# Kernel optimization log

Measured on AMD Instinct MI355X. Metric: run time of the kernel, lower is better.

## Reference

```python
import jax, jax.numpy as jnp
import numpy as np

P, O, Q, OS, M = 32, 128, 10, 256, 4
L, H, HD = 8, 16, 64
D = H * HD
DFF = 4 * D
ARIDX = 5
SEQ, HOR = 512, 256
EPS = 1e-6


def revin(x, mu, sigma, reverse):
    mu = mu[..., None]
    sg = sigma[..., None] + EPS
    return x * sg + mu if reverse else (x - mu) / sg


def update_stats(n, mu, sigma, x, mask):
    # Welford-style batched running stats; mask True = ignore.
    valid = (~mask).astype(x.dtype)
    k = valid.sum(-1)
    new_n = n + k
    safe = jnp.maximum(new_n, 1.0)
    new_mu = jnp.where(new_n > 0, (n * mu + (x * valid).sum(-1)) / safe, mu)
    M2 = n * sigma ** 2 + ((x - mu[:, None]) * (x - new_mu[:, None]) * valid).sum(-1)
    new_sigma = jnp.where(new_n > 0, jnp.sqrt(jnp.maximum(M2 / safe, 1e-12)), sigma)
    return new_n, new_mu, new_sigma


def running_stats(n, mu, sigma, patches, masks):
    # patches/masks: (B, N, P) -> scan over patch axis.
    def step(carry, pm):
        new = update_stats(carry[0], carry[1], carry[2], pm[0], pm[1])
        return new, (new[1], new[2])
    carry, (mus, sigs) = jax.lax.scan(
        step, (n, mu, sigma),
        (jnp.swapaxes(patches, 0, 1), jnp.swapaxes(masks, 0, 1)))
    return carry, jnp.swapaxes(mus, 0, 1), jnp.swapaxes(sigs, 0, 1)


def layer_norm(x, s):
    m = x.mean(-1, keepdims=True)
    v = ((x - m) ** 2).mean(-1, keepdims=True)
    return (x - m) * jax.lax.rsqrt(v + EPS) * s


def model_fwd(normed, mask, caches, prm):
    (W_in, b_in, ln1_s, Wqkv, Wo, ln2_s, W1, W2, lnf_s, Wout, Wqs) = prm
    B, N, _ = normed.shape
    feat = jnp.concatenate([normed, mask.astype(normed.dtype)], axis=-1)  # (B,N,2P)
    hdd = feat @ W_in + b_in
    new_caches = []
    for l in range(L):
        xn = layer_norm(hdd, ln1_s[l])
        qkv = (xn @ Wqkv[l]).reshape(B, N, 3, H, HD)
        q, k, v = qkv[:, :, 0], qkv[:, :, 1], qkv[:, :, 2]
        Kc = jnp.concatenate([caches[l][0], k], axis=1)
        Vc = jnp.concatenate([caches[l][1], v], axis=1)
        C = Kc.shape[1]
        off = C - N
        scores = jnp.einsum('bnhd,bmhd->bhnm', q, Kc) * (HD ** -0.5)
        allow = jnp.arange(C)[None, :] <= (jnp.arange(N)[:, None] + off)
        scores = jnp.where(allow[None, None], scores, -1e30)
        att = jax.nn.softmax(scores, axis=-1)
        out = jnp.einsum('bhnm,bmhd->bnhd', att, Vc).reshape(B, N, D) @ Wo[l]
        hdd = hdd + out
        hdd = hdd + jax.nn.gelu(layer_norm(hdd, ln2_s[l]) @ W1[l]) @ W2[l]
        new_caches.append((Kc, Vc))
    hf = layer_norm(hdd, lnf_s)
    return hf @ Wout, hf @ Wqs, new_caches


def decode(horizon, x, masks, prm):
    B, context = x.shape
    steps = (horizon - 1) // O
    npatch = context // P
    pi = x.reshape(B, npatch, P)
    pm = masks.reshape(B, npatch, P)
    z = jnp.zeros(B, x.dtype)
    (n, mu, sg), ctx_mu, ctx_sg = running_stats(z, z, z, pi, pm)
    caches = [(jnp.zeros((B, 0, H, HD), x.dtype), jnp.zeros((B, 0, H, HD), x.dtype)) for _ in range(L)]
    normed = jnp.where(pm, 0.0, revin(pi, ctx_mu, ctx_sg, False))
    no, nqs, caches = model_fwd(normed, pm, caches, prm)
    pf = revin(no, ctx_mu, ctx_sg, True).reshape(B, npatch, O, Q)
    qs = revin(nqs, ctx_mu, ctx_sg, True).reshape(B, npatch, OS, Q)[:, -1]
    ar = []
    last = pf[:, -1, :, ARIDX]
    for _ in range(steps):
        npi = last.reshape(B, M, P)
        nmask = jnp.zeros_like(npi, dtype=bool)
        (n, mu, sg), nmu, nsg = running_stats(n, mu, sg, npi, nmask)
        nnorm = revin(npi, nmu, nsg, False)
        no2, _, caches = model_fwd(nnorm, nmask, caches, prm)
        ren = revin(no2, nmu, nsg, True).reshape(B, M, O, Q)
        ar.append(ren[:, -1])
        last = ren[:, -1, :, ARIDX]
    ar_out = jnp.stack(ar, axis=1) if steps > 0 else None
    return pf, qs, ar_out


def flip_q(x):
    return jnp.concatenate([x[..., :1], x[..., 1:][..., ::-1]], axis=-1)


def compiled_decode(horizon, x, prm):
    B = x.shape[0]
    masks = jnp.zeros_like(x, dtype=bool)
    is_pos = jnp.all(x >= 0, axis=-1, keepdims=True)
    pf, qs, ar = decode(horizon, x, masks, prm)
    ff = jnp.concatenate([pf[:, -1], ar.reshape(B, -1, Q)], axis=1)
    fpf, fqs, far = decode(horizon, -x, masks, prm)
    fqs = flip_q(fqs)
    fpf = flip_q(fpf)
    fff = jnp.concatenate([fpf[:, -1], far.reshape(B, -1, Q)], axis=1)
    qs_c = (qs - fqs) / 2
    ff = (ff - fff) / 2
    idx = jnp.array([1, 2, 3, 4, 6, 7, 8, 9])
    ff = ff.at[:, :, idx].set(qs_c[:, :horizon, idx] - qs_c[:, :horizon, 5:6] + ff[:, :horizon, 5:6])
    ff = ff[:, :horizon]
    for i in [4, 3, 2, 1]:
        ff = ff.at[:, :, i].set(jnp.minimum(ff[:, :, i], ff[:, :, i + 1]))
    for i in [6, 7, 8, 9]:
        ff = ff.at[:, :, i].set(jnp.maximum(ff[:, :, i], ff[:, :, i - 1]))
    ff = jnp.where(is_pos[..., None], jnp.maximum(ff, 0.0), ff)
    return ff[..., 5], ff


def setup_inputs() -> dict:
    key = jax.random.key(0)
    ks = jax.random.split(key, 16)
    s = 0.02
    inp = {
        'inputs': jax.random.normal(ks[0], (32, SEQ, 1), dtype=jnp.float32),
        'W_in': jax.random.normal(ks[1], (2 * P, D), dtype=jnp.float32) * s,
        'b_in': jnp.zeros((D,), jnp.float32),
        'ln1_s': jnp.ones((L, D), jnp.float32),
        'Wqkv': jax.random.normal(ks[2], (L, D, 3 * D), dtype=jnp.float32) * s,
        'Wo': jax.random.normal(ks[3], (L, D, D), dtype=jnp.float32) * s,
        'ln2_s': jnp.ones((L, D), jnp.float32),
        'W1': jax.random.normal(ks[4], (L, D, DFF), dtype=jnp.float32) * s,
        'W2': jax.random.normal(ks[5], (L, DFF, D), dtype=jnp.float32) * s,
        'lnf_s': jnp.ones((D,), jnp.float32),
        'Wout': jax.random.normal(ks[6], (D, O * Q), dtype=jnp.float32) * s,
        'Wqs': jax.random.normal(ks[7], (D, OS * Q), dtype=jnp.float32) * s,
    }
    return inp


def reference(inputs, W_in, b_in, ln1_s, Wqkv, Wo, ln2_s, W1, W2, lnf_s, Wout, Wqs):
    prm = (W_in, b_in, ln1_s, Wqkv, Wo, ln2_s, W1, W2, lnf_s, Wout, Wqs)
    x = inputs[..., 0]  # squeeze(-1)
    med, _ = compiled_decode(HOR, x, prm)
    return med[..., None]  # (B, HOR, 1)
```

## Files before the change

kernel.cpp:

```cpp
#include <hip/hip_runtime.h>
#include <hip/hip_bf16.h>
#include <math.h>

#define PP 32
#define OO 128
#define QQ 10
#define MM 4
#define LL 8
#define HH 16
#define HD 64
#define DD 1024
#define DFF 4096
#define NPATCH 16
#define B2 64
#define CMAX 20
#define EPSF 1e-6f

typedef __attribute__((ext_vector_type(8))) short s16x8;
typedef __attribute__((ext_vector_type(4))) float f32x4;
typedef __hip_bfloat16 bf16;

__device__ inline float b2f(short u)
{
    return __uint_as_float(((unsigned)(unsigned short)u) << 16);
}

__device__ inline void ld_lds16(void* lds_base, const void* gaddr)
{
    __builtin_amdgcn_global_load_lds(
        (const __attribute__((address_space(1))) unsigned int*)gaddr,
        (__attribute__((address_space(3))) unsigned int*)lds_base, 16, 0, 0);
}

__global__ void stats_ctx_kernel(const float* __restrict__ x, float* __restrict__ ctx_mu,
                                 float* __restrict__ ctx_sg, float* __restrict__ ispos,
                                 float* __restrict__ normed)
{
    int b2 = blockIdx.x;
    int tid = threadIdx.x;
    float sign = (b2 < 32) ? 1.f : -1.f;
    const float* xp = x + (size_t)(b2 & 31) * 512;
    __shared__ float smu[NPATCH], ssg[NPATCH];
    if (tid == 0) {
        float n = 0.f, mu = 0.f, sg = 0.f;
        for (int t = 0; t < NPATCH; t++) {
            float s1 = 0.f;
            for (int p = 0; p < PP; p++) s1 += sign * xp[t * PP + p];
            float nn2 = n + 32.f;
            float nmu_ = (n * mu + s1) / nn2;
            float m2 = n * sg * sg;
            for (int p = 0; p < PP; p++) {
                float xv = sign * xp[t * PP + p];
                m2 += (xv - mu) * (xv - nmu_);
            }
            sg = sqrtf(fmaxf(m2 / nn2, 1e-12f));
            mu = nmu_; n = nn2;
            smu[t] = mu; ssg[t] = sg;
            ctx_mu[b2 * NPATCH + t] = mu;
            ctx_sg[b2 * NPATCH + t] = sg;
        }
        if (b2 < 32) {
            int ok = 1;
            for (int i = 0; i < 512; i++) if (xp[i] < 0.f) ok = 0;
            ispos[b2] = (float)ok;
        }
    }
    __syncthreads();
    for (int i = tid; i < 512; i += 64) {
        int t = i >> 5;
        normed[(size_t)b2 * 512 + i] = (sign * xp[i] - smu[t]) / (ssg[t] + EPSF);
    }
}

__global__ void stats_ar_kernel(const float* __restrict__ lastc, const float* __restrict__ ctx_mu,
                                const float* __restrict__ ctx_sg, float* __restrict__ nmu,
                                float* __restrict__ nsg, float* __restrict__ normed)
{
    int b2 = blockIdx.x;
    int tid = threadIdx.x;
    __shared__ float smu[MM], ssg[MM];
    const float* xp = lastc + (size_t)b2 * 128;
    if (tid == 0) {
        float n = 512.f;
        float mu = ctx_mu[b2 * NPATCH + 15];
        float sg = ctx_sg[b2 * NPATCH + 15];
        for (int t = 0; t < MM; t++) {
            float s1 = 0.f;
            for (int p = 0; p < PP; p++) s1 += xp[t * PP + p];
            float nn2 = n + 32.f;
            float nmu_ = (n * mu + s1) / nn2;
            float m2 = n * sg * sg;
            for (int p = 0; p < PP; p++) {
                float xv = xp[t * PP + p];
                m2 += (xv - mu) * (xv - nmu_);
            }
            sg = sqrtf(fmaxf(m2 / nn2, 1e-12f));
            mu = nmu_; n = nn2;
            smu[t] = mu; ssg[t] = sg;
            nmu[b2 * MM + t] = mu;
            nsg[b2 * MM + t] = sg;
        }
    }
    __syncthreads();
    for (int i = tid; i < 128; i += 64) {
        int t = i >> 5;
        normed[(size_t)b2 * 128 + i] = (xp[i] - smu[t]) / (ssg[t] + EPSF);
    }
}

__global__ __launch_bounds__(256) void embed_kernel(const float* __restrict__ normed,
                                                    const float* __restrict__ Win,
                                                    const float* __restrict__ bin,
                                                    float* __restrict__ hdd)
{
    int row = blockIdx.x;
    int tid = threadIdx.x;
    __shared__ float p[PP];
    if (tid < PP) p[tid] = normed[(size_t)row * PP + tid];
    __syncthreads();
    for (int c = tid; c < DD; c += 256) {
        float s = bin[c];
        for (int k = 0; k < PP; k++) s = fmaf(p[k], Win[k * DD + c], s);
        hdd[(size_t)row * DD + c] = s;
    }
}

__global__ __launch_bounds__(256) void layernorm_kernel(const float* __restrict__ in,
                                                        bf16* __restrict__ out,
                                                        const float* __restrict__ scale)
{
    int wave = threadIdx.x >> 6, lane = threadIdx.x & 63;
    size_t row = (size_t)blockIdx.x * 4 + wave;
    const float* x = in + row * DD + lane * 16;
    float e[16];
    #pragma unroll
    for (int j = 0; j < 4; j++) {
        float4 t = ((const float4*)x)[j];
        e[4 * j] = t.x; e[4 * j + 1] = t.y; e[4 * j + 2] = t.z; e[4 * j + 3] = t.w;
    }
    float s = 0.f;
    #pragma unroll
    for (int i = 0; i < 16; i++) s += e[i];
    #pragma unroll
    for (int o = 32; o > 0; o >>= 1) s += __shfl_xor(s, o, 64);
    float m = s * (1.f / 1024.f);
    float vv = 0.f;
    #pragma unroll
    for (int i = 0; i < 16; i++) { float d = e[i] - m; vv = fmaf(d, d, vv); }
    #pragma unroll
    for (int o = 32; o > 0; o >>= 1) vv += __shfl_xor(vv, o, 64);
    float inv = rsqrtf(vv * (1.f / 1024.f) + EPSF);
    const float* sc = scale + lane * 16;
    union { bf16 b[16]; s16x8 v2[2]; } ob;
    #pragma unroll
    for (int j = 0; j < 4; j++) {
        float4 t = ((const float4*)sc)[j];
        ob.b[4 * j]     = __float2bfloat16((e[4 * j]     - m) * inv * t.x);
        ob.b[4 * j + 1] = __float2bfloat16((e[4 * j + 1] - m) * inv * t.y);
        ob.b[4 * j + 2] = __float2bfloat16((e[4 * j + 2] - m) * inv * t.z);
        ob.b[4 * j + 3] = __float2bfloat16((e[4 * j + 3] - m) * inv * t.w);
    }
    s16x8* op = (s16x8*)(out + row * DD + lane * 16);
    op[0] = ob.v2[0]; op[1] = ob.v2[1];
}

__global__ __launch_bounds__(256) void transpose_w(const float* __restrict__ in,
                                                   bf16* __restrict__ out,
                                                   int R, int C)
{
    __shared__ float t[32][33];
    size_t base = (size_t)blockIdx.z * R * C;
    int c0 = blockIdx.x * 32, r0 = blockIdx.y * 32;
    int tx = threadIdx.x & 31, ty = threadIdx.x >> 5;
    #pragma unroll
    for (int s = 0; s < 4; s++)
        t[ty + 8 * s][tx] = in[base + (size_t)(r0 + ty + 8 * s) * C + c0 + tx];
    __syncthreads();
    #pragma unroll
    for (int s = 0; s < 4; s++)
        out[base + (size_t)(c0 + ty + 8 * s) * R + r0 + tx] = __float2bfloat16(t[tx][ty + 8 * s]);
}

__global__ void w5_kernel(const float* __restrict__ Wout, bf16* __restrict__ w5T)
{
    int i = blockIdx.x * 256 + threadIdx.x;
    int o = i >> 10, k = i & 1023;
    w5T[i] = __float2bfloat16(Wout[(size_t)k * (OO * QQ) + o * QQ + 5]);
}

__device__ inline float gelu_tanh(float x)
{
    float x3 = x * x * x;
    float t = tanhf(0.7978845608028654f * (x + 0.044715f * x3));
    return 0.5f * x * (1.f + t);
}

template<int BM, int BN, int EP>
__global__ __launch_bounds__(256) void hgemm(const bf16* __restrict__ A,
                                             const bf16* __restrict__ BT,
                                             float* __restrict__ C,
                                             bf16* __restrict__ Cbf,
                                             bf16* __restrict__ Kc,
                                             bf16* __restrict__ Vc,
                                             int M, int N, int K, int Kpart,
                                             int nn, int koff)
{
    constexpr int FM = BM / 32 > 0 ? BM / 32 : 1;
    constexpr int FN = BN / 32;
    __shared__ __align__(16) short As[BM * 64];
    __shared__ __align__(16) short Bs[BN * 64];
    int tid = threadIdx.x;
    int lane = tid & 63, wave = tid >> 6;
    int wm = (wave >> 1) * (BM / 2), wn = (wave & 1) * (BN / 2);
    int lm = lane & 15, quad = lane >> 4;
    int row0 = blockIdx.y * BM, col0 = blockIdx.x * BN;
    int kb = blockIdx.z * Kpart, ke = kb + Kpart;
    int r8 = lane >> 3;
    int gsw = ((lane & 7) ^ r8) * 8;
    int swz = lm & 7;

    f32x4 ac[FM][FN];
    #pragma unroll
    for (int i = 0; i < FM; i++)
        #pragma unroll
        for (int j = 0; j < FN; j++) ac[i][j] = (f32x4){0.f, 0.f, 0.f, 0.f};

    for (int k0 = kb; k0 < ke; k0 += 64) {
        #pragma unroll
        for (int c = 0; c < BM / 32; c++) {
            int ch = wave + 4 * c;
            ld_lds16(&As[ch * 512], A + (size_t)(row0 + ch * 8 + r8) * K + k0 + gsw);
        }
        #pragma unroll
        for (int c = 0; c < BN / 32; c++) {
            int ch = wave + 4 * c;
            ld_lds16(&Bs[ch * 512], BT + (size_t)(col0 + ch * 8 + r8) * K + k0 + gsw);
        }
        __syncthreads();
        #pragma unroll
        for (int kk = 0; kk < 2; kk++) {
            int gq = ((kk * 4 + quad) ^ swz) * 8;
            s16x8 af[FM], bfr[FN];
            #pragma unroll
            for (int i = 0; i < FM; i++) af[i] = *(const s16x8*)&As[(wm + i * 16 + lm) * 64 + gq];
            #pragma unroll
            for (int j = 0; j < FN; j++) bfr[j] = *(const s16x8*)&Bs[(wn + j * 16 + lm) * 64 + gq];
            #pragma unroll
            for (int i = 0; i < FM; i++)
                #pragma unroll
                for (int j = 0; j < FN; j++)
                    ac[i][j] = __builtin_amdgcn_mfma_f32_16x16x32_bf16(af[i], bfr[j], ac[i][j], 0, 0, 0);
        }
        __syncthreads();
    }
    bool multi = (gridDim.z > 1);
    #pragma unroll
    for (int i = 0; i < FM; i++) {
        #pragma unroll
        for (int j = 0; j < FN; j++) {
            #pragma unroll
            for (int r = 0; r < 4; r++) {
                int rr = row0 + wm + i * 16 + quad * 4 + r;
                int cc = col0 + wn + j * 16 + lm;
                float v = ac[i][j][r];
                if (EP == 0) {
                    size_t idx = (size_t)rr * N + cc;
                    if (multi) atomicAdd(&C[idx], v); else C[idx] = v;
                } else if (EP == 1) {
                    Cbf[(size_t)rr * N + cc] = __float2bfloat16(gelu_tanh(v));
                } else if (EP == 2) {
                    atomicAdd(&C[(size_t)rr * N + cc], v);
                } else {
                    if (cc < DD) {
                        C[(size_t)rr * DD + cc] = v;
                    } else {
                        int col = cc & (DD - 1);
                        int b = rr / nn, n = rr - b * nn;
                        int h = col >> 6, hd_ = col & 63;
                        size_t dst = (((size_t)(b * HH + h)) * CMAX + koff + n) * HD + hd_;
                        if (cc < 2 * DD) Kc[dst] = __float2bfloat16(v);
                        else             Vc[dst] = __float2bfloat16(v);
                    }
                }
            }
        }
    }
}

__global__ __launch_bounds__(64) void attn_kernel(const float* __restrict__ qb,
                                                  const bf16* __restrict__ Kc,
                                                  const bf16* __restrict__ Vc,
                                                  bf16* __restrict__ outb, int Nn, int off)
{
    int gid = blockIdx.x;
    int n = gid % Nn;
    int h = (gid / Nn) & (HH - 1);
    int b = gid / (Nn * HH);
    int lane = threadIdx.x;
    int len = n + off + 1;
    const float* q = qb + ((size_t)(b * Nn + n)) * DD + h * HD;
    const bf16* Kb = Kc + ((size_t)(b * HH + h)) * CMAX * HD;
    const bf16* Vb = Vc + ((size_t)(b * HH + h)) * CMAX * HD;

    __shared__ float sq[64];
    sq[lane] = q[lane];
    __syncthreads();

    float score = -1e30f;
    if (lane < len) {
        const s16x8* kr8 = (const s16x8*)(Kb + lane * HD);
        float s = 0.f;
        #pragma unroll
        for (int c = 0; c < 8; c++) {
            s16x8 kv = kr8[c];
            #pragma unroll
            for (int j = 0; j < 8; j++) s = fmaf(sq[c * 8 + j], b2f(kv[j]), s);
        }
        score = s * 0.125f;
    }
    float mx = score;
    for (int o = 32; o > 0; o >>= 1) mx = fmaxf(mx, __shfl_xor(mx, o, 64));
    float e = (lane < len) ? expf(score - mx) : 0.f;
    float sm = e;
    for (int o = 32; o > 0; o >>= 1) sm += __shfl_xor(sm, o, 64);
    float att = e / sm;
    __shared__ float satt[64];
    satt[lane] = att;
    __syncthreads();
    float acc = 0.f;
    for (int m = 0; m < len; m++) acc = fmaf(satt[m], __bfloat162float(Vb[m * HD + lane]), acc);
    outb[((size_t)(b * Nn + n)) * DD + h * HD + lane] = __float2bfloat16(acc);
}

__global__ __launch_bounds__(128) void lnout5_kernel(const float* __restrict__ hdd,
                                                     const float* __restrict__ lnf,
                                                     const bf16* __restrict__ w5T,
                                                     const float* __restrict__ mus,
                                                     const float* __restrict__ sgs,
                                                     float* __restrict__ last, int Nn)
{
    int b2 = blockIdx.x, tid = threadIdx.x;
    const float* x = hdd + (size_t)(b2 * Nn + Nn - 1) * DD;
    __shared__ float sx[DD];
    __shared__ float red[128];
    float s = 0.f;
    for (int i = tid; i < DD; i += 128) s += x[i];
    red[tid] = s; __syncthreads();
    for (int st = 64; st > 0; st >>= 1) { if (tid < st) red[tid] += red[tid + st]; __syncthreads(); }
    float m = red[0] * (1.f / 1024.f);
    __syncthreads();
    float vv = 0.f;
    for (int i = tid; i < DD; i += 128) { float d = x[i] - m; vv = fmaf(d, d, vv); }
    red[tid] = vv; __syncthreads();
    for (int st = 64; st > 0; st >>= 1) { if (tid < st) red[tid] += red[tid + st]; __syncthreads(); }
    float inv = rsqrtf(red[0] * (1.f / 1024.f) + EPSF);
    __syncthreads();
    for (int i = tid; i < DD; i += 128) sx[i] = (x[i] - m) * inv * lnf[i];
    __syncthreads();
    const s16x8* w8 = (const s16x8*)(w5T + (size_t)tid * DD);
    float acc = 0.f;
    for (int k = 0; k < DD / 8; k++) {
        s16x8 wv = w8[k];
        #pragma unroll
        for (int j = 0; j < 8; j++) acc = fmaf(sx[k * 8 + j], b2f(wv[j]), acc);
    }
    float mu = mus[b2 * Nn + (Nn - 1)];
    float sg = sgs[b2 * Nn + (Nn - 1)];
    last[(size_t)b2 * 128 + tid] = acc * (sg + EPSF) + mu;
}

__global__ void combine_kernel(const float* __restrict__ lastc, const float* __restrict__ lasta,
                               const float* __restrict__ ispos, float* __restrict__ out)
{
    int i = blockIdx.x * 256 + threadIdx.x;
    int b = i >> 8, t = i & 255;
    float a, an;
    if (t < 128) { a = lastc[b * 128 + t];        an = lastc[(b + 32) * 128 + t]; }
    else         { a = lasta[b * 128 + t - 128];  an = lasta[(b + 32) * 128 + t - 128]; }
    float raw = (a - an) * 0.5f;
    if (ispos[b] > 0.5f) raw = fmaxf(raw, 0.f);
    out[i] = raw;
}

extern "C" void kernel_launch(void* const* d_in, const int* in_sizes, int n_in,
                              void* d_out, int out_size, void* d_ws, size_t ws_size,
                              hipStream_t stream)
{
    (void)in_sizes; (void)n_in; (void)out_size;
    const float* x     = (const float*)d_in[0];
    const float* W_in  = (const float*)d_in[1];
    const float* b_in  = (const float*)d_in[2];
    const float* ln1_s = (const float*)d_in[3];
    const float* Wqkv  = (const float*)d_in[4];
    const float* Wo    = (const float*)d_in[5];
    const float* ln2_s = (const float*)d_in[6];
    const float* W1    = (const float*)d_in[7];
    const float* W2    = (const float*)d_in[8];
    const float* lnf_s = (const float*)d_in[9];
    const float* Wout  = (const float*)d_in[10];
    float* out = (float*)d_out;

    size_t off = 0;
    auto alloc = [&](size_t bytes) {
        char* p = (char*)d_ws + off;
        off = (off + bytes + 255) & ~(size_t)255;
        return (void*)p;
    };
    float* ctx_mu = (float*)alloc(B2 * NPATCH * 4);
    float* ctx_sg = (float*)alloc(B2 * NPATCH * 4);
    float* nmu    = (float*)alloc(B2 * MM * 4);
    float* nsg    = (float*)alloc(B2 * MM * 4);
    float* ispos  = (float*)alloc(32 * 4);
    float* normed = (float*)alloc(B2 * NPATCH * PP * 4);
    float* lastc  = (float*)alloc(B2 * 128 * 4);
    float* lasta  = (float*)alloc(B2 * 128 * 4);
    float* hdd    = (float*)alloc((size_t)B2 * NPATCH * DD * 4);
    float* qb     = (float*)alloc((size_t)B2 * NPATCH * DD * 4);
    bf16* xn      = (bf16*)alloc((size_t)B2 * NPATCH * DD * 2);
    bf16* attnb   = (bf16*)alloc((size_t)B2 * NPATCH * DD * 2);
    bf16* ffnb    = (bf16*)alloc((size_t)B2 * NPATCH * DFF * 2);
    const size_t cache_l = (size_t)B2 * HH * CMAX * HD;
    bf16* kcache  = (bf16*)alloc(LL * cache_l * 2);
    bf16* vcache  = (bf16*)alloc(LL * cache_l * 2);
    bf16* w5T     = (bf16*)alloc((size_t)OO * DD * 2);

    const size_t szQKV = (size_t)DD * 3 * DD;
    const size_t szWO  = (size_t)DD * DD;
    const size_t szW1  = (size_t)DD * DFF;
    const size_t szW2  = (size_t)DFF * DD;
    const size_t WBYTES = (szQKV + szWO + szW1 + szW2) * LL * 2 + 4096;
    bool big = (off + WBYTES) <= ws_size;

    bf16 *wqkvT = nullptr, *woT = nullptr, *w1T = nullptr, *w2T = nullptr, *rot = nullptr;
    if (big) {
        wqkvT = (bf16*)alloc(LL * szQKV * 2);
        woT   = (bf16*)alloc(LL * szWO * 2);
        w1T   = (bf16*)alloc(LL * szW1 * 2);
        w2T   = (bf16*)alloc(LL * szW2 * 2);
        transpose_w<<<dim3(3072 / 32, 1024 / 32, LL), 256, 0, stream>>>(Wqkv, wqkvT, 1024, 3072);
        transpose_w<<<dim3(1024 / 32, 1024 / 32, LL), 256, 0, stream>>>(Wo, woT, 1024, 1024);
        transpose_w<<<dim3(4096 / 32, 1024 / 32, LL), 256, 0, stream>>>(W1, w1T, 1024, 4096);
        transpose_w<<<dim3(1024 / 32, 4096 / 32, LL), 256, 0, stream>>>(W2, w2T, 4096, 1024);
    } else {
        rot = (bf16*)alloc(szW1 * 2);
    }
    w5_kernel<<<(OO * DD) / 256, 256, 0, stream>>>(Wout, w5T);

    stats_ctx_kernel<<<B2, 64, 0, stream>>>(x, ctx_mu, ctx_sg, ispos, normed);
    {
        const int R = B2 * NPATCH;
        embed_kernel<<<R, 256, 0, stream>>>(normed, W_in, b_in, hdd);
        for (int l = 0; l < LL; l++) {
            bf16* kc = kcache + l * cache_l;
            bf16* vc = vcache + l * cache_l;
            layernorm_kernel<<<R / 4, 256, 0, stream>>>(hdd, xn, ln1_s + l * DD);
            bf16* bq;
            if (big) bq = wqkvT + l * szQKV;
            else { transpose_w<<<dim3(96, 32, 1), 256, 0, stream>>>(Wqkv + l * szQKV, rot, 1024, 3072); bq = rot; }
            hgemm<64, 128, 3><<<dim3(24, 16, 1), 256, 0, stream>>>(xn, bq, qb, nullptr, kc, vc,
                                                                   R, 3072, 1024, 1024, NPATCH, 0);
            attn_kernel<<<B2 * HH * NPATCH, 64, 0, stream>>>(qb, kc, vc, attnb, NPATCH, 0);
            bf16* bo;
            if (big) bo = woT + l * szWO;
            else { transpose_w<<<dim3(32, 32, 1), 256, 0, stream>>>(Wo + l * szWO, rot, 1024, 1024); bo = rot; }
            hgemm<64, 64, 2><<<dim3(16, 16, 2), 256, 0, stream>>>(attnb, bo, hdd, nullptr, nullptr, nullptr,
                                                                  R, 1024, 1024, 512, 0, 0);
            layernorm_kernel<<<R / 4, 256, 0, stream>>>(hdd, xn, ln2_s + l * DD);
            bf16* b1;
            if (big) b1 = w1T + l * szW1;
            else { transpose_w<<<dim3(128, 32, 1), 256, 0, stream>>>(W1 + l * szW1, rot, 1024, 4096); b1 = rot; }
            hgemm<64, 128, 1><<<dim3(32, 16, 1), 256, 0, stream>>>(xn, b1, nullptr, ffnb, nullptr, nullptr,
                                                                   R, 4096, 1024, 1024, 0, 0);
            bf16* bw2;
            if (big) bw2 = w2T + l * szW2;
            else { transpose_w<<<dim3(32, 128, 1), 256, 0, stream>>>(W2 + l * szW2, rot, 4096, 1024); bw2 = rot; }
            hgemm<64, 64, 2><<<dim3(16, 16, 4), 256, 0, stream>>>(ffnb, bw2, hdd, nullptr, nullptr, nullptr,
                                                                  R, 1024, 4096, 1024, 0, 0);
        }
        lnout5_kernel<<<B2, 128, 0, stream>>>(hdd, lnf_s, w5T, ctx_mu, ctx_sg, lastc, NPATCH);
    }

    stats_ar_kernel<<<B2, 64, 0, stream>>>(lastc, ctx_mu, ctx_sg, nmu, nsg, normed);
    {
        const int R = B2 * MM;
        embed_kernel<<<R, 256, 0, stream>>>(normed, W_in, b_in, hdd);
        for (int l = 0; l < LL; l++) {
            bf16* kc = kcache + l * cache_l;
            bf16* vc = vcache + l * cache_l;
            layernorm_kernel<<<R / 4, 256, 0, stream>>>(hdd, xn, ln1_s + l * DD);
            bf16* bq;
            if (big) bq = wqkvT + l * szQKV;
            else { transpose_w<<<dim3(96, 32, 1), 256, 0, stream>>>(Wqkv + l * szQKV, rot, 1024, 3072); bq = rot; }
            hgemm<32, 64, 3><<<dim3(48, 8, 1), 256, 0, stream>>>(xn, bq, qb, nullptr, kc, vc,
                                                                 R, 3072, 1024, 1024, MM, NPATCH);
            attn_kernel<<<B2 * HH * MM, 64, 0, stream>>>(qb, kc, vc, attnb, MM, NPATCH);
            bf16* bo;
            if (big) bo = woT + l * szWO;
            else { transpose_w<<<dim3(32, 32, 1), 256, 0, stream>>>(Wo + l * szWO, rot, 1024, 1024); bo = rot; }
            hgemm<32, 64, 2><<<dim3(16, 8, 2), 256, 0, stream>>>(attnb, bo, hdd, nullptr, nullptr, nullptr,
                                                                 R, 1024, 1024, 512, 0, 0);
            layernorm_kernel<<<R / 4, 256, 0, stream>>>(hdd, xn, ln2_s + l * DD);
            bf16* b1;
            if (big) b1 = w1T + l * szW1;
            else { transpose_w<<<dim3(128, 32, 1), 256, 0, stream>>>(W1 + l * szW1, rot, 1024, 4096); b1 = rot; }
            hgemm<32, 128, 1><<<dim3(32, 8, 1), 256, 0, stream>>>(xn, b1, nullptr, ffnb, nullptr, nullptr,
                                                                  R, 4096, 1024, 1024, 0, 0);
            bf16* bw2;
            if (big) bw2 = w2T + l * szW2;
            else { transpose_w<<<dim3(32, 128, 1), 256, 0, stream>>>(W2 + l * szW2, rot, 4096, 1024); bw2 = rot; }
            hgemm<32, 64, 2><<<dim3(16, 8, 4), 256, 0, stream>>>(ffnb, bw2, hdd, nullptr, nullptr, nullptr,
                                                                 R, 1024, 4096, 1024, 0, 0);
        }
        lnout5_kernel<<<B2, 128, 0, stream>>>(hdd, lnf_s, w5T, nmu, nsg, lasta, MM);
    }

    combine_kernel<<<(32 * 256) / 256, 256, 0, stream>>>(lastc, lasta, ispos, out);
}
```

Measured before the change: 1.938 ms.

## Fuse layernorm into GEMM A-loads and fold LN scales into weights

Removes the standalone layernorm kernels. A new hgemm_ln computes per-row mean and rstd inside the GEMM block and normalizes the fp32 activations on the fly while staging them to shared memory as bf16. The LN scale vectors (ln1, ln2, lnf) are folded into the transposed weight matrices during preprocessing, and the attention kernel now packs four heads per 256-thread block. This saves kernel launches and the bf16 xn round trip through memory. In exchange, every column block recomputes the row statistics and reads fp32 activations instead of bf16, so A-side traffic rises.

```diff
diff --git a/kernel.cpp b/kernel.cpp
--- a/kernel.cpp
+++ b/kernel.cpp
@@ -125,67 +125,33 @@
     }
 }
 
-__global__ __launch_bounds__(256) void layernorm_kernel(const float* __restrict__ in,
-                                                        bf16* __restrict__ out,
-                                                        const float* __restrict__ scale)
-{
-    int wave = threadIdx.x >> 6, lane = threadIdx.x & 63;
-    size_t row = (size_t)blockIdx.x * 4 + wave;
-    const float* x = in + row * DD + lane * 16;
-    float e[16];
-    #pragma unroll
-    for (int j = 0; j < 4; j++) {
-        float4 t = ((const float4*)x)[j];
-        e[4 * j] = t.x; e[4 * j + 1] = t.y; e[4 * j + 2] = t.z; e[4 * j + 3] = t.w;
-    }
-    float s = 0.f;
-    #pragma unroll
-    for (int i = 0; i < 16; i++) s += e[i];
-    #pragma unroll
-    for (int o = 32; o > 0; o >>= 1) s += __shfl_xor(s, o, 64);
-    float m = s * (1.f / 1024.f);
-    float vv = 0.f;
-    #pragma unroll
-    for (int i = 0; i < 16; i++) { float d = e[i] - m; vv = fmaf(d, d, vv); }
-    #pragma unroll
-    for (int o = 32; o > 0; o >>= 1) vv += __shfl_xor(vv, o, 64);
-    float inv = rsqrtf(vv * (1.f / 1024.f) + EPSF);
-    const float* sc = scale + lane * 16;
-    union { bf16 b[16]; s16x8 v2[2]; } ob;
-    #pragma unroll
-    for (int j = 0; j < 4; j++) {
-        float4 t = ((const float4*)sc)[j];
-        ob.b[4 * j]     = __float2bfloat16((e[4 * j]     - m) * inv * t.x);
-        ob.b[4 * j + 1] = __float2bfloat16((e[4 * j + 1] - m) * inv * t.y);
-        ob.b[4 * j + 2] = __float2bfloat16((e[4 * j + 2] - m) * inv * t.z);
-        ob.b[4 * j + 3] = __float2bfloat16((e[4 * j + 3] - m) * inv * t.w);
-    }
-    s16x8* op = (s16x8*)(out + row * DD + lane * 16);
-    op[0] = ob.v2[0]; op[1] = ob.v2[1];
-}
-
 __global__ __launch_bounds__(256) void transpose_w(const float* __restrict__ in,
                                                    bf16* __restrict__ out,
-                                                   int R, int C)
+                                                   int R, int C,
+                                                   const float* __restrict__ scl)
 {
     __shared__ float t[32][33];
     size_t base = (size_t)blockIdx.z * R * C;
     int c0 = blockIdx.x * 32, r0 = blockIdx.y * 32;
     int tx = threadIdx.x & 31, ty = threadIdx.x >> 5;
     #pragma unroll
-    for (int s = 0; s < 4; s++)
-        t[ty + 8 * s][tx] = in[base + (size_t)(r0 + ty + 8 * s) * C + c0 + tx];
+    for (int s = 0; s < 4; s++) {
+        int row = r0 + ty + 8 * s;
+        float sc = scl ? scl[(size_t)blockIdx.z * R + row] : 1.f;
+        t[ty + 8 * s][tx] = in[base + (size_t)row * C + c0 + tx] * sc;
+    }
     __syncthreads();
     #pragma unroll
     for (int s = 0; s < 4; s++)
         out[base + (size_t)(c0 + ty + 8 * s) * R + r0 + tx] = __float2bfloat16(t[tx][ty + 8 * s]);
 }
 
-__global__ void w5_kernel(const float* __restrict__ Wout, bf16* __restrict__ w5T)
+__global__ void w5_kernel(const float* __restrict__ Wout, const float* __restrict__ lnf,
+                          bf16* __restrict__ w5T)
 {
     int i = blockIdx.x * 256 + threadIdx.x;
     int o = i >> 10, k = i & 1023;
-    w5T[i] = __float2bfloat16(Wout[(size_t)k * (OO * QQ) + o * QQ + 5]);
+    w5T[i] = __float2bfloat16(Wout[(size_t)k * (OO * QQ) + o * QQ + 5] * lnf[k]);
 }
 
 __device__ inline float gelu_tanh(float x)
@@ -200,10 +166,7 @@
                                              const bf16* __restrict__ BT,
                                              float* __restrict__ C,
                                              bf16* __restrict__ Cbf,
-                                             bf16* __restrict__ Kc,
-                                             bf16* __restrict__ Vc,
-                                             int M, int N, int K, int Kpart,
-                                             int nn, int koff)
+                                             int M, int N, int K, int Kpart)
 {
     constexpr int FM = BM / 32 > 0 ? BM / 32 : 1;
     constexpr int FN = BN / 32;
@@ -253,7 +216,6 @@
         }
         __syncthreads();
     }
-    bool multi = (gridDim.z > 1);
     #pragma unroll
     for (int i = 0; i < FM; i++) {
         #pragma unroll
@@ -263,13 +225,126 @@
                 int rr = row0 + wm + i * 16 + quad * 4 + r;
                 int cc = col0 + wn + j * 16 + lm;
                 float v = ac[i][j][r];
-                if (EP == 0) {
-                    size_t idx = (size_t)rr * N + cc;
-                    if (multi) atomicAdd(&C[idx], v); else C[idx] = v;
-                } else if (EP == 1) {
+                if (EP == 1) Cbf[(size_t)rr * N + cc] = __float2bfloat16(gelu_tanh(v));
+                else         atomicAdd(&C[(size_t)rr * N + cc], v);
+            }
+        }
+    }
+}
+
+template<int BM, int BN, int EP>
+__global__ __launch_bounds__(256) void hgemm_ln(const float* __restrict__ Afp,
+                                                const bf16* __restrict__ BT,
+                                                float* __restrict__ C,
+                                                bf16* __restrict__ Cbf,
+                                                bf16* __restrict__ Kc,
+                                                bf16* __restrict__ Vc,
+                                                int M, int N, int K,
+                                                int nn, int koff)
+{
+    constexpr int FM = BM / 32 > 0 ? BM / 32 : 1;
+    constexpr int FN = BN / 32;
+    constexpr int TPR = 256 / BM;
+    constexpr int FPT = 64 / TPR;
+    __shared__ __align__(16) short As[BM * 64];
+    __shared__ __align__(16) short Bs[BN * 64];
+    __shared__ float sa[BM], sb[BM];
+    int tid = threadIdx.x;
+    int lane = tid & 63, wave = tid >> 6;
+    int wm = (wave >> 1) * (BM / 2), wn = (wave & 1) * (BN / 2);
+    int lm = lane & 15, quad = lane >> 4;
+    int row0 = blockIdx.y * BM, col0 = blockIdx.x * BN;
+    int r8 = lane >> 3;
+    int gsw = ((lane & 7) ^ r8) * 8;
+    int swz = lm & 7;
+
+    for (int r = wave; r < BM; r += 4) {
+        const float* xr = Afp + (size_t)(row0 + r) * K + lane * 16;
+        float e[16];
+        #pragma unroll
+        for (int j = 0; j < 4; j++) {
+            float4 t = ((const float4*)xr)[j];
+            e[4 * j] = t.x; e[4 * j + 1] = t.y; e[4 * j + 2] = t.z; e[4 * j + 3] = t.w;
+        }
+        float s = 0.f;
+        #pragma unroll
+        for (int i = 0; i < 16; i++) s += e[i];
+        #pragma unroll
+        for (int o = 32; o > 0; o >>= 1) s += __shfl_xor(s, o, 64);
+        float m = s * (1.f / 1024.f);
+        float vv = 0.f;
+        #pragma unroll
+        for (int i = 0; i < 16; i++) { float d = e[i] - m; vv = fmaf(d, d, vv); }
+        #pragma unroll
+        for (int o = 32; o > 0; o >>= 1) vv += __shfl_xor(vv, o, 64);
+        if (lane == 0) {
+            float inv = rsqrtf(vv * (1.f / 1024.f) + EPSF);
+            sa[r] = inv; sb[r] = -m * inv;
+        }
+    }
+    __syncthreads();
+    int arow = tid / TPR;
+    int acol = (tid % TPR) * FPT;
+    float ia = sa[arow], ib = sb[arow];
+    const float* ap = Afp + (size_t)(row0 + arow) * K + acol;
+    int g0 = (tid % TPR) * (FPT / 8);
+
+    f32x4 ac[FM][FN];
+    #pragma unroll
+    for (int i = 0; i < FM; i++)
+        #pragma unroll
+        for (int j = 0; j < FN; j++) ac[i][j] = (f32x4){0.f, 0.f, 0.f, 0.f};
+
+    for (int k0 = 0; k0 < K; k0 += 64) {
+        float4 f[FPT / 4];
+        #pragma unroll
+        for (int j = 0; j < FPT / 4; j++) f[j] = ((const float4*)(ap + k0))[j];
+        union { bf16 h[16]; s16x8 v[2]; } pk;
+        #pragma unroll
+        for (int j = 0; j < FPT / 4; j++) {
+            pk.h[4 * j + 0] = __float2bfloat16(fmaf(f[j].x, ia, ib));
+            pk.h[4 * j + 1] = __float2bfloat16(fmaf(f[j].y, ia, ib));
+            pk.h[4 * j + 2] = __float2bfloat16(fmaf(f[j].z, ia, ib));
+            pk.h[4 * j + 3] = __float2bfloat16(fmaf(f[j].w, ia, ib));
+        }
+        #pragma unroll
+        for (int g = 0; g < FPT / 8; g++) {
+            int gg = (g0 + g) ^ (arow & 7);
+            *(s16x8*)&As[arow * 64 + gg * 8] = pk.v[g];
+        }
+        #pragma unroll
+        for (int c = 0; c < BN / 32; c++) {
+            int ch = wave + 4 * c;
+            ld_lds16(&Bs[ch * 512], BT + (size_t)(col0 + ch * 8 + r8) * K + k0 + gsw);
+        }
+        __syncthreads();
+        #pragma unroll
+        for (int kk = 0; kk < 2; kk++) {
+            int gq = ((kk * 4 + quad) ^ swz) * 8;
+            s16x8 af[FM], bfr[FN];
+            #pragma unroll
+            for (int i = 0; i < FM; i++) af[i] = *(const s16x8*)&As[(wm + i * 16 + lm) * 64 + gq];
+            #pragma unroll
+            for (int j = 0; j < FN; j++) bfr[j] = *(const s16x8*)&Bs[(wn + j * 16 + lm) * 64 + gq];
+            #pragma unroll
+            for (int i = 0; i < FM; i++)
+                #pragma unroll
+                for (int j = 0; j < FN; j++)
+                    ac[i][j] = __builtin_amdgcn_mfma_f32_16x16x32_bf16(af[i], bfr[j], ac[i][j], 0, 0, 0);
+        }
+        __syncthreads();
+    }
+    #pragma unroll
+    for (int i = 0; i < FM; i++) {
+        #pragma unroll
+        for (int j = 0; j < FN; j++) {
+            #pragma unroll
+            for (int r = 0; r < 4; r++) {
+                int rr = row0 + wm + i * 16 + quad * 4 + r;
+                int cc = col0 + wn + j * 16 + lm;
+                float v = ac[i][j][r];
+                if (EP == 1) {
                     Cbf[(size_t)rr * N + cc] = __float2bfloat16(gelu_tanh(v));
-                } else if (EP == 2) {
-                    atomicAdd(&C[(size_t)rr * N + cc], v);
                 } else {
                     if (cc < DD) {
                         C[(size_t)rr * DD + cc] = v;
@@ -287,23 +362,24 @@
     }
 }
 
-__global__ __launch_bounds__(64) void attn_kernel(const float* __restrict__ qb,
-                                                  const bf16* __restrict__ Kc,
-                                                  const bf16* __restrict__ Vc,
-                                                  bf16* __restrict__ outb, int Nn, int off)
-{
-    int gid = blockIdx.x;
+__global__ __launch_bounds__(256) void attn_kernel(const float* __restrict__ qb,
+                                                   const bf16* __restrict__ Kc,
+                                                   const bf16* __restrict__ Vc,
+                                                   bf16* __restrict__ outb, int Nn, int off)
+{
+    int wave = threadIdx.x >> 6, lane = threadIdx.x & 63;
+    int gid = blockIdx.x * 4 + wave;
     int n = gid % Nn;
     int h = (gid / Nn) & (HH - 1);
     int b = gid / (Nn * HH);
-    int lane = threadIdx.x;
     int len = n + off + 1;
     const float* q = qb + ((size_t)(b * Nn + n)) * DD + h * HD;
     const bf16* Kb = Kc + ((size_t)(b * HH + h)) * CMAX * HD;
     const bf16* Vb = Vc + ((size_t)(b * HH + h)) * CMAX * HD;
 
-    __shared__ float sq[64];
-    sq[lane] = q[lane];
+    __shared__ float sq[4][64];
+    __shared__ float satt[4][64];
+    sq[wave][lane] = q[lane];
     __syncthreads();
 
     float score = -1e30f;
@@ -314,7 +390,7 @@
         for (int c = 0; c < 8; c++) {
             s16x8 kv = kr8[c];
             #pragma unroll
-            for (int j = 0; j < 8; j++) s = fmaf(sq[c * 8 + j], b2f(kv[j]), s);
+            for (int j = 0; j < 8; j++) s = fmaf(sq[wave][c * 8 + j], b2f(kv[j]), s);
         }
         score = s * 0.125f;
     }
@@ -323,17 +399,14 @@
     float e = (lane < len) ? expf(score - mx) : 0.f;
     float sm = e;
     for (int o = 32; o > 0; o >>= 1) sm += __shfl_xor(sm, o, 64);
-    float att = e / sm;
-    __shared__ float satt[64];
-    satt[lane] = att;
+    satt[wave][lane] = e / sm;
     __syncthreads();
     float acc = 0.f;
-    for (int m = 0; m < len; m++) acc = fmaf(satt[m], __bfloat162float(Vb[m * HD + lane]), acc);
+    for (int m = 0; m < len; m++) acc = fmaf(satt[wave][m], __bfloat162float(Vb[m * HD + lane]), acc);
     outb[((size_t)(b * Nn + n)) * DD + h * HD + lane] = __float2bfloat16(acc);
 }
 
 __global__ __launch_bounds__(128) void lnout5_kernel(const float* __restrict__ hdd,
-                                                     const float* __restrict__ lnf,
                                                      const bf16* __restrict__ w5T,
                                                      const float* __restrict__ mus,
                                                      const float* __restrict__ sgs,
@@ -355,7 +428,7 @@
     for (int st = 64; st > 0; st >>= 1) { if (tid < st) red[tid] += red[tid + st]; __syncthreads(); }
     float inv = rsqrtf(red[0] * (1.f / 1024.f) + EPSF);
     __syncthreads();
-    for (int i = tid; i < DD; i += 128) sx[i] = (x[i] - m) * inv * lnf[i];
+    for (int i = tid; i < DD; i += 128) sx[i] = (x[i] - m) * inv;
     __syncthreads();
     const s16x8* w8 = (const s16x8*)(w5T + (size_t)tid * DD);
     float acc = 0.f;
@@ -416,7 +489,6 @@
     float* lasta  = (float*)alloc(B2 * 128 * 4);
     float* hdd    = (float*)alloc((size_t)B2 * NPATCH * DD * 4);
     float* qb     = (float*)alloc((size_t)B2 * NPATCH * DD * 4);
-    bf16* xn      = (bf16*)alloc((size_t)B2 * NPATCH * DD * 2);
     bf16* attnb   = (bf16*)alloc((size_t)B2 * NPATCH * DD * 2);
     bf16* ffnb    = (bf16*)alloc((size_t)B2 * NPATCH * DFF * 2);
     const size_t cache_l = (size_t)B2 * HH * CMAX * HD;
@@ -437,14 +509,14 @@
         woT   = (bf16*)alloc(LL * szWO * 2);
         w1T   = (bf16*)alloc(LL * szW1 * 2);
         w2T   = (bf16*)alloc(LL * szW2 * 2);
-        transpose_w<<<dim3(3072 / 32, 1024 / 32, LL), 256, 0, stream>>>(Wqkv, wqkvT, 1024, 3072);
-        transpose_w<<<dim3(1024 / 32, 1024 / 32, LL), 256, 0, stream>>>(Wo, woT, 1024, 1024);
-        transpose_w<<<dim3(4096 / 32, 1024 / 32, LL), 256, 0, stream>>>(W1, w1T, 1024, 4096);
-        transpose_w<<<dim3(1024 / 32, 4096 / 32, LL), 256, 0, stream>>>(W2, w2T, 4096, 1024);
+        transpose_w<<<dim3(3072 / 32, 1024 / 32, LL), 256, 0, stream>>>(Wqkv, wqkvT, 1024, 3072, ln1_s);
+        transpose_w<<<dim3(1024 / 32, 1024 / 32, LL), 256, 0, stream>>>(Wo, woT, 1024, 1024, nullptr);
+        transpose_w<<<dim3(4096 / 32, 1024 / 32, LL), 256, 0, stream>>>(W1, w1T, 1024, 4096, ln2_s);
+        transpose_w<<<dim3(1024 / 32, 4096 / 32, LL), 256, 0, stream>>>(W2, w2T, 4096, 1024, nullptr);
     } else {
         rot = (bf16*)alloc(szW1 * 2);
     }
-    w5_kernel<<<(OO * DD) / 256, 256, 0, stream>>>(Wout, w5T);
+    w5_kernel<<<(OO * DD) / 256, 256, 0, stream>>>(Wout, lnf_s, w5T);
 
     stats_ctx_kernel<<<B2, 64, 0, stream>>>(x, ctx_mu, ctx_sg, ispos, normed);
     {
@@ -453,31 +525,29 @@
         for (int l = 0; l < LL; l++) {
             bf16* kc = kcache + l * cache_l;
             bf16* vc = vcache + l * cache_l;
-            layernorm_kernel<<<R / 4, 256, 0, stream>>>(hdd, xn, ln1_s + l * DD);
             bf16* bq;
             if (big) bq = wqkvT + l * szQKV;
-            else { transpose_w<<<dim3(96, 32, 1), 256, 0, stream>>>(Wqkv + l * szQKV, rot, 1024, 3072); bq = rot; }
-            hgemm<64, 128, 3><<<dim3(24, 16, 1), 256, 0, stream>>>(xn, bq, qb, nullptr, kc, vc,
-                                                                   R, 3072, 1024, 1024, NPATCH, 0);
-            attn_kernel<<<B2 * HH * NPATCH, 64, 0, stream>>>(qb, kc, vc, attnb, NPATCH, 0);
+            else { transpose_w<<<dim3(96, 32, 1), 256, 0, stream>>>(Wqkv + l * szQKV, rot, 1024, 3072, ln1_s + l * DD); bq = rot; }
+            hgemm_ln<64, 128, 3><<<dim3(24, 16, 1), 256, 0, stream>>>(hdd, bq, qb, nullptr, kc, vc,
+                                                                      R, 3072, 1024, NPATCH, 0);
+            attn_kernel<<<B2 * HH * NPATCH / 4, 256, 0, stream>>>(qb, kc, vc, attnb, NPATCH, 0);
             bf16* bo;
             if (big) bo = woT + l * szWO;
-            else { transpose_w<<<dim3(32, 32, 1), 256, 0, stream>>>(Wo + l * szWO, rot, 1024, 1024); bo = rot; }
-            hgemm<64, 64, 2><<<dim3(16, 16, 2), 256, 0, stream>>>(attnb, bo, hdd, nullptr, nullptr, nullptr,
-                                                                  R, 1024, 1024, 512, 0, 0);
-            layernorm_kernel<<<R / 4, 256, 0, stream>>>(hdd, xn, ln2_s + l * DD);
+            else { transpose_w<<<dim3(32, 32, 1), 256, 0, stream>>>(Wo + l * szWO, rot, 1024, 1024, nullptr); bo = rot; }
+            hgemm<64, 64, 2><<<dim3(16, 16, 2), 256, 0, stream>>>(attnb, bo, hdd, nullptr,
+                                                                  R, 1024, 1024, 512);
             bf16* b1;
             if (big) b1 = w1T + l * szW1;
-            else { transpose_w<<<dim3(128, 32, 1), 256, 0, stream>>>(W1 + l * szW1, rot, 1024, 4096); b1 = rot; }
-            hgemm<64, 128, 1><<<dim3(32, 16, 1), 256, 0, stream>>>(xn, b1, nullptr, ffnb, nullptr, nullptr,
-                                                                   R, 4096, 1024, 1024, 0, 0);
+            else { transpose_w<<<dim3(128, 32, 1), 256, 0, stream>>>(W1 + l * szW1, rot, 1024, 4096, ln2_s + l * DD); b1 = rot; }
+            hgemm_ln<64, 128, 1><<<dim3(32, 16, 1), 256, 0, stream>>>(hdd, b1, nullptr, ffnb, nullptr, nullptr,
+                                                                      R, 4096, 1024, 0, 0);
             bf16* bw2;
             if (big) bw2 = w2T + l * szW2;
-            else { transpose_w<<<dim3(32, 128, 1), 256, 0, stream>>>(W2 + l * szW2, rot, 4096, 1024); bw2 = rot; }
-            hgemm<64, 64, 2><<<dim3(16, 16, 4), 256, 0, stream>>>(ffnb, bw2, hdd, nullptr, nullptr, nullptr,
-                                                                  R, 1024, 4096, 1024, 0, 0);
-        }
-        lnout5_kernel<<<B2, 128, 0, stream>>>(hdd, lnf_s, w5T, ctx_mu, ctx_sg, lastc, NPATCH);
+            else { transpose_w<<<dim3(32, 128, 1), 256, 0, stream>>>(W2 + l * szW2, rot, 4096, 1024, nullptr); bw2 = rot; }
+            hgemm<64, 64, 2><<<dim3(16, 16, 4), 256, 0, stream>>>(ffnb, bw2, hdd, nullptr,
+                                                                  R, 1024, 4096, 1024);
+        }
+        lnout5_kernel<<<B2, 128, 0, stream>>>(hdd, w5T, ctx_mu, ctx_sg, lastc, NPATCH);
     }
 
     stats_ar_kernel<<<B2, 64, 0, stream>>>(lastc, ctx_mu, ctx_sg, nmu, nsg, normed);
@@ -487,31 +557,29 @@
         for (int l = 0; l < LL; l++) {
             bf16* kc = kcache + l * cache_l;
             bf16* vc = vcache + l * cache_l;
-            layernorm_kernel<<<R / 4, 256, 0, stream>>>(hdd, xn, ln1_s + l * DD);
             bf16* bq;
             if (big) bq = wqkvT + l * szQKV;
-            else { transpose_w<<<dim3(96, 32, 1), 256, 0, stream>>>(Wqkv + l * szQKV, rot, 1024, 3072); bq = rot; }
-            hgemm<32, 64, 3><<<dim3(48, 8, 1), 256, 0, stream>>>(xn, bq, qb, nullptr, kc, vc,
-                                                                 R, 3072, 1024, 1024, MM, NPATCH);
-            attn_kernel<<<B2 * HH * MM, 64, 0, stream>>>(qb, kc, vc, attnb, MM, NPATCH);
+            else { transpose_w<<<dim3(96, 32, 1), 256, 0, stream>>>(Wqkv + l * szQKV, rot, 1024, 3072, ln1_s + l * DD); bq = rot; }
+            hgemm_ln<32, 64, 3><<<dim3(48, 8, 1), 256, 0, stream>>>(hdd, bq, qb, nullptr, kc, vc,
+                                                                    R, 3072, 1024, MM, NPATCH);
+            attn_kernel<<<B2 * HH * MM / 4, 256, 0, stream>>>(qb, kc, vc, attnb, MM, NPATCH);
             bf16* bo;
             if (big) bo = woT + l * szWO;
-            else { transpose_w<<<dim3(32, 32, 1), 256, 0, stream>>>(Wo + l * szWO, rot, 1024, 1024); bo = rot; }
-            hgemm<32, 64, 2><<<dim3(16, 8, 2), 256, 0, stream>>>(attnb, bo, hdd, nullptr, nullptr, nullptr,
-                                                                 R, 1024, 1024, 512, 0, 0);
-            layernorm_kernel<<<R / 4, 256, 0, stream>>>(hdd, xn, ln2_s + l * DD);
+            else { transpose_w<<<dim3(32, 32, 1), 256, 0, stream>>>(Wo + l * szWO, rot, 1024, 1024, nullptr); bo = rot; }
+            hgemm<32, 64, 2><<<dim3(16, 8, 2), 256, 0, stream>>>(attnb, bo, hdd, nullptr,
+                                                                 R, 1024, 1024, 512);
             bf16* b1;
             if (big) b1 = w1T + l * szW1;
-            else { transpose_w<<<dim3(128, 32, 1), 256, 0, stream>>>(W1 + l * szW1, rot, 1024, 4096); b1 = rot; }
-            hgemm<32, 128, 1><<<dim3(32, 8, 1), 256, 0, stream>>>(xn, b1, nullptr, ffnb, nullptr, nullptr,
-                                                                  R, 4096, 1024, 1024, 0, 0);
+            else { transpose_w<<<dim3(128, 32, 1), 256, 0, stream>>>(W1 + l * szW1, rot, 1024, 4096, ln2_s + l * DD); b1 = rot; }
+            hgemm_ln<32, 128, 1><<<dim3(32, 8, 1), 256, 0, stream>>>(hdd, b1, nullptr, ffnb, nullptr, nullptr,
+                                                                     R, 4096, 1024, 0, 0);
             bf16* bw2;
             if (big) bw2 = w2T + l * szW2;
-            else { transpose_w<<<dim3(32, 128, 1), 256, 0, stream>>>(W2 + l * szW2, rot, 4096, 1024); bw2 = rot; }
-            hgemm<32, 64, 2><<<dim3(16, 8, 4), 256, 0, stream>>>(ffnb, bw2, hdd, nullptr, nullptr, nullptr,
-                                                                 R, 1024, 4096, 1024, 0, 0);
-        }
-        lnout5_kernel<<<B2, 128, 0, stream>>>(hdd, lnf_s, w5T, nmu, nsg, lasta, MM);
+            else { transpose_w<<<dim3(32, 128, 1), 256, 0, stream>>>(W2 + l * szW2, rot, 4096, 1024, nullptr); bw2 = rot; }
+            hgemm<32, 64, 2><<<dim3(16, 8, 4), 256, 0, stream>>>(ffnb, bw2, hdd, nullptr,
+                                                                 R, 1024, 4096, 1024);
+        }
+        lnout5_kernel<<<B2, 128, 0, stream>>>(hdd, w5T, nmu, nsg, lasta, MM);
     }
 
     combine_kernel<<<(32 * 256) / 256, 256, 0, stream>>>(lastc, lasta, ispos, out);
```

Measured after the change: 2.195 ms. +13.2%, slower.
